# Performance work log

Hardware: AMD Instinct MI355X
Metric: run time of the kernel (lower is better)

## Reference

```python
import jax, jax.numpy as jnp
import numpy as np

N, E, D = 100000, 640000, 128

def setup_inputs() -> dict:
    key = jax.random.key(0)
    ks = jax.random.split(key, 12)
    s = 1.0 / np.sqrt(D)
    sg = 1.0 / np.sqrt(2 * D)
    return {
        "nodes": jax.random.normal(ks[0], (N, D), jnp.float32),
        "globals_": jax.random.normal(ks[1], (1, D), jnp.float32),
        "senders": jax.random.randint(ks[2], (E,), 0, N, jnp.int32),
        "receivers": jax.random.randint(ks[3], (E,), 0, N, jnp.int32),
        "W1_w": jax.random.normal(ks[4], (D, D), jnp.float32) * s,
        "W1_b": jnp.zeros((D,), jnp.float32),
        "W2_w": jax.random.normal(ks[5], (D, D), jnp.float32) * s,
        "W2_b": jnp.zeros((D,), jnp.float32),
        "W3_w": jax.random.normal(ks[6], (D, D), jnp.float32) * s,
        "W3_b": jnp.zeros((D,), jnp.float32),
        "Wg_w": jax.random.normal(ks[7], (2 * D, D), jnp.float32) * sg,
        "Wg_b": jnp.zeros((D,), jnp.float32),
    }


def reference(nodes, globals_, senders, receivers,
              W1_w, W1_b, W2_w, W2_b, W3_w, W3_b, Wg_w, Wg_b):
    n = nodes.shape[0]
    # W1 skip-branch projection
    h = nodes @ W1_w + W1_b                              # [N, D]
    # GraphConvolution: W2 projection + symmetric-normalized sum aggregation
    conv = nodes @ W2_w + W2_b                           # [N, D]
    ones = jnp.ones(senders.shape, conv.dtype)
    send_deg = jax.ops.segment_sum(ones, senders, num_segments=n)
    recv_deg = jax.ops.segment_sum(ones, receivers, num_segments=n)
    conv = conv * jax.lax.rsqrt(jnp.maximum(send_deg, 1.0))[:, None]
    agg = jax.ops.segment_sum(conv[senders], receivers, num_segments=n)  # gather + scatter
    agg = agg * jax.lax.rsqrt(jnp.maximum(recv_deg, 1.0))[:, None]
    h = h + agg
    # global -> node broadcast (globals is not None)
    h = h + (globals_[0:1] @ W3_w + W3_b)
    h = jax.nn.relu(h)
    h = h + nodes                                        # residual
    # global update: aggregate nodes (sum over single graph) + gated residual
    an = jnp.sum(h, axis=0, keepdims=True)               # [1, D]
    g_new = globals_ + jax.nn.relu(jnp.concatenate([an, globals_], axis=-1) @ Wg_w + Wg_b)
    return h, g_new
```

## Files before the change

### kernel.cpp

```cpp
#include <hip/hip_runtime.h>

#define D 128
#define SCH 1024
#define AGGB 2048

typedef __attribute__((ext_vector_type(8))) short short8;
typedef __attribute__((ext_vector_type(4))) float floatx4;

__device__ inline void bf16split(float x, ushort& hi, ushort& lo) {
  unsigned u = __float_as_uint(x);
  unsigned rh = (u + 0x7FFFu + ((u >> 16) & 1u)) & 0xFFFF0000u;
  hi = (ushort)(rh >> 16);
  float fl = x - __uint_as_float(rh);
  unsigned ul = __float_as_uint(fl);
  lo = (ushort)((ul + 0x7FFFu + ((ul >> 16) & 1u)) >> 16);
}

__global__ void k_front(const int* __restrict__ snd, const int* __restrict__ rcv,
                        int* __restrict__ cs, int* __restrict__ cr, int E, int nbE,
                        const float* __restrict__ g, const float* __restrict__ W3,
                        const float* __restrict__ b3, float* __restrict__ gvec) {
  __shared__ float part[256];
  if ((int)blockIdx.x < nbE) {
    const int e = blockIdx.x * 256 + threadIdx.x;
    if (e < E) {
      atomicAdd(cs + snd[e], 1);
      atomicAdd(cr + rcv[e], 1);
    }
    return;
  }
  const int j = threadIdx.x & 127, half = threadIdx.x >> 7;
  float acc = 0.f;
  for (int k = half * 64; k < half * 64 + 64; ++k)
    acc = fmaf(g[k], W3[k * D + j], acc);
  part[threadIdx.x] = acc;
  __syncthreads();
  if (threadIdx.x < D) gvec[j] = b3[j] + part[j] + part[j + 128];
}

__global__ void k_scan(const int* __restrict__ cnt, int* __restrict__ bsum,
                       int* __restrict__ off, int* __restrict__ cursor, int n) {
  __shared__ int sh[256];
  __shared__ int red[4];
  const int t = threadIdx.x, b = blockIdx.x;
  const int base = b * SCH + t * 4;
  int4 v = make_int4(0, 0, 0, 0);
  if (base < n) v = *(const int4*)(cnt + base);
  const int s = v.x + v.y + v.z + v.w;
  sh[t] = s;
  __syncthreads();
  for (int st = 1; st < 256; st <<= 1) {
    const int u = (t >= st) ? sh[t - st] : 0;
    __syncthreads();
    sh[t] += u;
    __syncthreads();
  }
  if (t == 255) atomicExch(bsum + b, sh[255] + 1);
  int pre = 0;
  if (t < b) {
    int x = atomicAdd(bsum + t, 0);
    while (x == 0) {
      __builtin_amdgcn_s_sleep(1);
      x = atomicAdd(bsum + t, 0);
    }
    pre = x - 1;
  }
#pragma unroll
  for (int o = 32; o > 0; o >>= 1) pre += __shfl_down(pre, o, 64);
  if ((t & 63) == 0) red[t >> 6] = pre;
  __syncthreads();
  const int gbase = red[0] + red[1] + red[2] + red[3];
  const int ex = sh[t] - s + gbase;
  if (base < n) {
    const int4 o4 = make_int4(ex, ex + v.x, ex + v.x + v.y, ex + v.x + v.y + v.z);
    *(int4*)(off + base) = o4;
    *(int4*)(cursor + base) = o4;
  }
}

__global__ void k_fill(const int* __restrict__ snd, const int* __restrict__ rcv,
                       int* __restrict__ cursor, int* __restrict__ srt, int E) {
  const int e = blockIdx.x * blockDim.x + threadIdx.x;
  if (e < E) {
    const int p = atomicAdd(cursor + rcv[e], 1);
    srt[p] = snd[e];
  }
}

__global__ __launch_bounds__(256) void k_agg(
    const float* __restrict__ nodes, const int* __restrict__ off,
    int* __restrict__ cnt_recv, const int* __restrict__ cnt_send,
    const int* __restrict__ srt, ushort* __restrict__ yh,
    ushort* __restrict__ yl, int n, const float* __restrict__ W1,
    const float* __restrict__ W2, ushort* __restrict__ wt) {
  if ((int)blockIdx.x >= AGGB) {
    const int id = ((int)blockIdx.x - AGGB) * 256 + threadIdx.x;
    const int mat = id >> 14, idx = id & 16383;
    const int k = idx >> 7, nn = idx & 127;
    const float x = (mat ? W2 : W1)[k * D + nn];
    ushort hi, lo;
    bf16split(x, hi, lo);
    wt[(size_t)mat * 32768 + (size_t)nn * 128 + k] = hi;
    wt[(size_t)mat * 32768 + 16384 + (size_t)nn * 128 + k] = lo;
    return;
  }
  float* cf = (float*)cnt_recv;
  const int hw = threadIdx.x >> 5, ln = threadIdx.x & 31;
  const int ghw = blockIdx.x * 8 + hw;
  const int nhw = AGGB * 8;
  const int c0 = ln * 4;

  for (int r0 = ghw; r0 < n; r0 += 2 * nhw) {
    const int r1 = r0 + nhw;
    const bool has1 = r1 < n;
    const int dg0 = cnt_recv[r0];
    const int o0 = off[r0];
    const int dg1 = has1 ? cnt_recv[r1] : 0;
    const int o1 = has1 ? off[r1] : o0;
    const int safe0 = (dg0 > 0) ? o0 : 0;
    const int safe1 = (dg1 > 0) ? o1 : 0;

    int idx0[8], idx1[8];
#pragma unroll
    for (int j = 0; j < 8; ++j) {
      idx0[j] = srt[safe0 + (j < dg0 ? j : 0)];
      idx1[j] = srt[safe1 + (j < dg1 ? j : 0)];
    }
    float4 g0[8], g1[8];
#pragma unroll
    for (int j = 0; j < 8; ++j)
      g0[j] = *(const float4*)(nodes + (size_t)idx0[j] * D + c0);
#pragma unroll
    for (int j = 0; j < 8; ++j)
      g1[j] = *(const float4*)(nodes + (size_t)idx1[j] * D + c0);
    float rs0[8], rs1[8];
#pragma unroll
    for (int j = 0; j < 8; ++j) {
      rs0[j] = (j < dg0) ? rsqrtf(fmaxf((float)cnt_send[idx0[j]], 1.f)) : 0.f;
      rs1[j] = (j < dg1) ? rsqrtf(fmaxf((float)cnt_send[idx1[j]], 1.f)) : 0.f;
    }

    float sx0 = 0.f, sy0 = 0.f, sz0 = 0.f, sw0 = 0.f, cs0 = 0.f;
    float sx1 = 0.f, sy1 = 0.f, sz1 = 0.f, sw1 = 0.f, cs1 = 0.f;
#pragma unroll
    for (int j = 0; j < 8; ++j) {
      sx0 = fmaf(rs0[j], g0[j].x, sx0);
      sy0 = fmaf(rs0[j], g0[j].y, sy0);
      sz0 = fmaf(rs0[j], g0[j].z, sz0);
      sw0 = fmaf(rs0[j], g0[j].w, sw0);
      cs0 += rs0[j];
      sx1 = fmaf(rs1[j], g1[j].x, sx1);
      sy1 = fmaf(rs1[j], g1[j].y, sy1);
      sz1 = fmaf(rs1[j], g1[j].z, sz1);
      sw1 = fmaf(rs1[j], g1[j].w, sw1);
      cs1 += rs1[j];
    }
    for (int i = 8; i < dg0; ++i) {
      const int s = srt[o0 + i];
      const float r = rsqrtf(fmaxf((float)cnt_send[s], 1.f));
      const float4 c = *(const float4*)(nodes + (size_t)s * D + c0);
      sx0 = fmaf(r, c.x, sx0); sy0 = fmaf(r, c.y, sy0);
      sz0 = fmaf(r, c.z, sz0); sw0 = fmaf(r, c.w, sw0);
      cs0 += r;
    }
    for (int i = 8; i < dg1; ++i) {
      const int s = srt[o1 + i];
      const float r = rsqrtf(fmaxf((float)cnt_send[s], 1.f));
      const float4 c = *(const float4*)(nodes + (size_t)s * D + c0);
      sx1 = fmaf(r, c.x, sx1); sy1 = fmaf(r, c.y, sy1);
      sz1 = fmaf(r, c.z, sz1); sw1 = fmaf(r, c.w, sw1);
      cs1 += r;
    }

    {
      const float rr = rsqrtf(fmaxf((float)dg0, 1.f));
      ushort h0, l0, h1, l1, h2, l2, h3, l3;
      bf16split(sx0 * rr, h0, l0);
      bf16split(sy0 * rr, h1, l1);
      bf16split(sz0 * rr, h2, l2);
      bf16split(sw0 * rr, h3, l3);
      *(ushort4*)(yh + (size_t)r0 * D + c0) = make_ushort4(h0, h1, h2, h3);
      *(ushort4*)(yl + (size_t)r0 * D + c0) = make_ushort4(l0, l1, l2, l3);
      if (ln == 0) cf[r0] = rr * cs0;
    }
    if (has1) {
      const float rr = rsqrtf(fmaxf((float)dg1, 1.f));
      ushort h0, l0, h1, l1, h2, l2, h3, l3;
      bf16split(sx1 * rr, h0, l0);
      bf16split(sy1 * rr, h1, l1);
      bf16split(sz1 * rr, h2, l2);
      bf16split(sw1 * rr, h3, l3);
      *(ushort4*)(yh + (size_t)r1 * D + c0) = make_ushort4(h0, h1, h2, h3);
      *(ushort4*)(yl + (size_t)r1 * D + c0) = make_ushort4(l0, l1, l2, l3);
      if (ln == 0) cf[r1] = rr * cs1;
    }
  }
}

__global__ __launch_bounds__(256, 2) void k_gemm(
    const float* __restrict__ A, const ushort* __restrict__ yh,
    const ushort* __restrict__ yl, const ushort* __restrict__ wt,
    const float* __restrict__ b1, const float* __restrict__ b2,
    const float* __restrict__ gvec, const float* __restrict__ cf,
    float* __restrict__ outH, float* __restrict__ an, int n) {
  __shared__ ushort A1h[64 * 40], A1l[64 * 40], A2h[64 * 40], A2l[64 * 40];
  __shared__ ushort Wh[256 * 40], Wl[256 * 40];
  const int t = threadIdx.x;
  const int row0 = blockIdx.x * 64;
  const int lane = t & 63, w = t >> 6;
  const int m = lane & 15, quad = lane >> 4;

  floatx4 acc[4][2];
#pragma unroll
  for (int i = 0; i < 4; ++i)
#pragma unroll
    for (int j = 0; j < 2; ++j) acc[i][j] = (floatx4)0.f;

  const int arow = t >> 2, akl = (t & 3) * 8;
  const int wcol = t, wmat = wcol >> 7, wn = wcol & 127;
  const int grow = row0 + arow;
  const bool ok = grow < n;

  for (int p = 0; p < 4; ++p) {
    {
      const float* gp = A + (size_t)grow * D + p * 32 + akl;
      float4 v0 = make_float4(0.f, 0.f, 0.f, 0.f), v1 = v0;
      if (ok) {
        v0 = *(const float4*)gp;
        v1 = *(const float4*)(gp + 4);
      }
      ushort h0, l0, h1, l1, h2, l2, h3, l3;
      const int a = arow * 40 + akl;
      bf16split(v0.x, h0, l0); bf16split(v0.y, h1, l1);
      bf16split(v0.z, h2, l2); bf16split(v0.w, h3, l3);
      *(ushort4*)&A1h[a] = make_ushort4(h0, h1, h2, h3);
      *(ushort4*)&A1l[a] = make_ushort4(l0, l1, l2, l3);
      bf16split(v1.x, h0, l0); bf16split(v1.y, h1, l1);
      bf16split(v1.z, h2, l2); bf16split(v1.w, h3, l3);
      *(ushort4*)&A1h[a + 4] = make_ushort4(h0, h1, h2, h3);
      *(ushort4*)&A1l[a + 4] = make_ushort4(l0, l1, l2, l3);
    }
    if (ok) {
      const int a = arow * 40 + akl;
      *(uint4*)&A2h[a] = *(const uint4*)(yh + (size_t)grow * D + p * 32 + akl);
      *(uint4*)&A2l[a] = *(const uint4*)(yl + (size_t)grow * D + p * 32 + akl);
    }
    {
      const ushort* gh = wt + (size_t)wmat * 32768 + (size_t)wn * 128 + p * 32;
      const ushort* gl = gh + 16384;
      const int a = wcol * 40;
#pragma unroll
      for (int c = 0; c < 4; ++c) {
        *(uint4*)&Wh[a + 8 * c] = *(const uint4*)(gh + 8 * c);
        *(uint4*)&Wl[a + 8 * c] = *(const uint4*)(gl + 8 * c);
      }
    }
    __syncthreads();
    short8 a1h[4], a1l[4], a2h[4], a2l[4];
#pragma unroll
    for (int i = 0; i < 4; ++i) {
      const int r = (i * 16 + m) * 40 + quad * 8;
      a1h[i] = *(const short8*)&A1h[r];
      a1l[i] = *(const short8*)&A1l[r];
      a2h[i] = *(const short8*)&A2h[r];
      a2l[i] = *(const short8*)&A2l[r];
    }
#pragma unroll
    for (int j = 0; j < 2; ++j) {
      const int r1 = (w * 32 + j * 16 + m) * 40 + quad * 8;
      const int r2 = (128 + w * 32 + j * 16 + m) * 40 + quad * 8;
      const short8 w1h = *(const short8*)&Wh[r1];
      const short8 w1l = *(const short8*)&Wl[r1];
      const short8 w2h = *(const short8*)&Wh[r2];
      const short8 w2l = *(const short8*)&Wl[r2];
#pragma unroll
      for (int i = 0; i < 4; ++i) {
        floatx4 c = acc[i][j];
        c = __builtin_amdgcn_mfma_f32_16x16x32_bf16(a1h[i], w1h, c, 0, 0, 0);
        c = __builtin_amdgcn_mfma_f32_16x16x32_bf16(a1h[i], w1l, c, 0, 0, 0);
        c = __builtin_amdgcn_mfma_f32_16x16x32_bf16(a1l[i], w1h, c, 0, 0, 0);
        c = __builtin_amdgcn_mfma_f32_16x16x32_bf16(a2h[i], w2h, c, 0, 0, 0);
        c = __builtin_amdgcn_mfma_f32_16x16x32_bf16(a2h[i], w2l, c, 0, 0, 0);
        c = __builtin_amdgcn_mfma_f32_16x16x32_bf16(a2l[i], w2h, c, 0, 0, 0);
        acc[i][j] = c;
      }
    }
    __syncthreads();
  }

  float bb[2], b2c[2];
#pragma unroll
  for (int j = 0; j < 2; ++j) {
    const int col = w * 32 + j * 16 + m;
    bb[j] = b1[col] + gvec[col];
    b2c[j] = b2[col];
  }
  float asum[2] = {0.f, 0.f};
#pragma unroll
  for (int i = 0; i < 4; ++i)
#pragma unroll
    for (int pp = 0; pp < 4; ++pp) {
      const int rg = row0 + i * 16 + quad * 4 + pp;
      if (rg >= n) continue;
      const float crv = cf[rg];
#pragma unroll
      for (int j = 0; j < 2; ++j) {
        const int col = w * 32 + j * 16 + m;
        float v = acc[i][j][pp] + bb[j] + crv * b2c[j];
        v = fmaxf(v, 0.f) + A[(size_t)rg * D + col];
        outH[(size_t)rg * D + col] = v;
        asum[j] += v;
      }
    }
#pragma unroll
  for (int j = 0; j < 2; ++j) {
    float v = asum[j];
    v += __shfl_xor(v, 16);
    v += __shfl_xor(v, 32);
    if (lane < 16) atomicAdd(an + w * 32 + j * 16 + m, v);
  }
}

__global__ void k_gupdate(const float* __restrict__ an, const float* __restrict__ g,
                          const float* __restrict__ Wg, const float* __restrict__ bg,
                          float* __restrict__ gout) {
  __shared__ float part[256];
  const int j = threadIdx.x & 127, half = threadIdx.x >> 7;
  float acc = 0.f;
  if (half == 0) {
    for (int k = 0; k < D; ++k) acc = fmaf(an[k], Wg[k * D + j], acc);
  } else {
    for (int k = 0; k < D; ++k) acc = fmaf(g[k], Wg[(D + k) * D + j], acc);
  }
  part[threadIdx.x] = acc;
  __syncthreads();
  if (threadIdx.x < D)
    gout[j] = g[j] + fmaxf(bg[j] + part[j] + part[j + 128], 0.f);
}

extern "C" void kernel_launch(void* const* d_in, const int* in_sizes, int n_in,
                              void* d_out, int out_size, void* d_ws, size_t ws_size,
                              hipStream_t stream) {
  const float* nodes = (const float*)d_in[0];
  const float* globals_ = (const float*)d_in[1];
  const int* senders = (const int*)d_in[2];
  const int* receivers = (const int*)d_in[3];
  const float* W1_w = (const float*)d_in[4];
  const float* W1_b = (const float*)d_in[5];
  const float* W2_w = (const float*)d_in[6];
  const float* W2_b = (const float*)d_in[7];
  const float* W3_w = (const float*)d_in[8];
  const float* W3_b = (const float*)d_in[9];
  const float* Wg_w = (const float*)d_in[10];
  const float* Wg_b = (const float*)d_in[11];
  const int N = in_sizes[0] / D;
  const int E = in_sizes[2];
  const int nb = (N + SCH - 1) / SCH;
  const int nbE = (E + 255) / 256;

  float* h = (float*)d_out;
  float* gout = h + (size_t)N * D;

  float* ws = (float*)d_ws;
  ushort* yh = (ushort*)ws;
  ushort* yl = yh + (size_t)N * D;
  int* cnt_send = (int*)(yl + (size_t)N * D);
  int* cnt_recv = cnt_send + N;
  int* bsum = cnt_recv + N;
  float* an = (float*)(bsum + 256);
  int* off = (int*)(an + D);
  int* cursor = off + N;
  int* srt = cursor + N;
  float* gvec = (float*)(srt + E);
  ushort* wt = (ushort*)cursor;

  (void)hipMemsetAsync(cnt_send, 0, (size_t)(2 * N + 256 + D) * sizeof(int), stream);

  hipLaunchKernelGGL(k_front, dim3(nbE + 1), dim3(256), 0, stream,
                     senders, receivers, cnt_send, cnt_recv, E, nbE,
                     globals_, W3_w, W3_b, gvec);
  hipLaunchKernelGGL(k_scan, dim3(nb), dim3(256), 0, stream,
                     cnt_recv, bsum, off, cursor, N);
  hipLaunchKernelGGL(k_fill, dim3(nbE), dim3(256), 0, stream,
                     senders, receivers, cursor, srt, E);
  hipLaunchKernelGGL(k_agg, dim3(AGGB + 128), dim3(256), 0, stream,
                     nodes, off, cnt_recv, cnt_send, srt, yh, yl, N,
                     W1_w, W2_w, wt);
  hipLaunchKernelGGL(k_gemm, dim3((N + 63) / 64), dim3(256), 0, stream,
                     nodes, yh, yl, wt, W1_b, W2_b, gvec,
                     (const float*)cnt_recv, h, an, N);
  hipLaunchKernelGGL(k_gupdate, dim3(1), dim3(256), 0, stream, an, globals_,
                     Wg_w, Wg_b, gout);
}
```

Baseline: 362.9 us.

## Pre-split nodes to bf16 hi/lo and drop LDS staging in GEMM

```diff
diff --git a/kernel.cpp b/kernel.cpp
--- a/kernel.cpp
+++ b/kernel.cpp
@@ -19,23 +19,45 @@
 __global__ void k_front(const int* __restrict__ snd, const int* __restrict__ rcv,
                         int* __restrict__ cs, int* __restrict__ cr, int E, int nbE,
                         const float* __restrict__ g, const float* __restrict__ W3,
-                        const float* __restrict__ b3, float* __restrict__ gvec) {
+                        const float* __restrict__ b3, float* __restrict__ gvec,
+                        const float* __restrict__ nodes, ushort* __restrict__ nhl,
+                        int n) {
   __shared__ float part[256];
-  if ((int)blockIdx.x < nbE) {
-    const int e = blockIdx.x * 256 + threadIdx.x;
+  const int b = blockIdx.x;
+  if (b < nbE) {
+    const int e = b * 256 + threadIdx.x;
     if (e < E) {
       atomicAdd(cs + snd[e], 1);
       atomicAdd(cr + rcv[e], 1);
     }
     return;
   }
-  const int j = threadIdx.x & 127, half = threadIdx.x >> 7;
-  float acc = 0.f;
-  for (int k = half * 64; k < half * 64 + 64; ++k)
-    acc = fmaf(g[k], W3[k * D + j], acc);
-  part[threadIdx.x] = acc;
-  __syncthreads();
-  if (threadIdx.x < D) gvec[j] = b3[j] + part[j] + part[j + 128];
+  if (b == nbE) {
+    const int j = threadIdx.x & 127, half = threadIdx.x >> 7;
+    float acc = 0.f;
+    for (int k = half * 64; k < half * 64 + 64; ++k)
+      acc = fmaf(g[k], W3[k * D + j], acc);
+    part[threadIdx.x] = acc;
+    __syncthreads();
+    if (threadIdx.x < D) gvec[j] = b3[j] + part[j] + part[j + 128];
+    return;
+  }
+  const int id = (b - nbE - 1) * 256 + threadIdx.x;
+  if (id >= n * 16) return;
+  const int r = id >> 4, c = (id & 15) * 8;
+  const float* gp = nodes + (size_t)r * D + c;
+  const float4 v0 = *(const float4*)gp;
+  const float4 v1 = *(const float4*)(gp + 4);
+  ushort h0, l0, h1, l1, h2, l2, h3, l3;
+  ushort* ob = nhl + (size_t)r * 256;
+  bf16split(v0.x, h0, l0); bf16split(v0.y, h1, l1);
+  bf16split(v0.z, h2, l2); bf16split(v0.w, h3, l3);
+  *(ushort4*)(ob + c) = make_ushort4(h0, h1, h2, h3);
+  *(ushort4*)(ob + 128 + c) = make_ushort4(l0, l1, l2, l3);
+  bf16split(v1.x, h0, l0); bf16split(v1.y, h1, l1);
+  bf16split(v1.z, h2, l2); bf16split(v1.w, h3, l3);
+  *(ushort4*)(ob + c + 4) = make_ushort4(h0, h1, h2, h3);
+  *(ushort4*)(ob + 128 + c + 4) = make_ushort4(l0, l1, l2, l3);
 }
 
 __global__ void k_scan(const int* __restrict__ cnt, int* __restrict__ bsum,
@@ -197,14 +219,12 @@
   }
 }
 
-__global__ __launch_bounds__(256, 2) void k_gemm(
-    const float* __restrict__ A, const ushort* __restrict__ yh,
+__global__ __launch_bounds__(256, 3) void k_gemm(
+    const float* __restrict__ A, const ushort* nhl, const ushort* __restrict__ yh,
     const ushort* __restrict__ yl, const ushort* __restrict__ wt,
     const float* __restrict__ b1, const float* __restrict__ b2,
     const float* __restrict__ gvec, const float* __restrict__ cf,
-    float* __restrict__ outH, float* __restrict__ an, int n) {
-  __shared__ ushort A1h[64 * 40], A1l[64 * 40], A2h[64 * 40], A2l[64 * 40];
-  __shared__ ushort Wh[256 * 40], Wl[256 * 40];
+    float* outH, float* __restrict__ an, int n) {
   const int t = threadIdx.x;
   const int row0 = blockIdx.x * 64;
   const int lane = t & 63, w = t >> 6;
@@ -216,63 +236,30 @@
 #pragma unroll
     for (int j = 0; j < 2; ++j) acc[i][j] = (floatx4)0.f;
 
-  const int arow = t >> 2, akl = (t & 3) * 8;
-  const int wcol = t, wmat = wcol >> 7, wn = wcol & 127;
-  const int grow = row0 + arow;
-  const bool ok = grow < n;
+  int rr[4];
+#pragma unroll
+  for (int i = 0; i < 4; ++i) rr[i] = min(row0 + i * 16 + m, n - 1);
 
   for (int p = 0; p < 4; ++p) {
-    {
-      const float* gp = A + (size_t)grow * D + p * 32 + akl;
-      float4 v0 = make_float4(0.f, 0.f, 0.f, 0.f), v1 = v0;
-      if (ok) {
-        v0 = *(const float4*)gp;
-        v1 = *(const float4*)(gp + 4);
-      }
-      ushort h0, l0, h1, l1, h2, l2, h3, l3;
-      const int a = arow * 40 + akl;
-      bf16split(v0.x, h0, l0); bf16split(v0.y, h1, l1);
-      bf16split(v0.z, h2, l2); bf16split(v0.w, h3, l3);
-      *(ushort4*)&A1h[a] = make_ushort4(h0, h1, h2, h3);
-      *(ushort4*)&A1l[a] = make_ushort4(l0, l1, l2, l3);
-      bf16split(v1.x, h0, l0); bf16split(v1.y, h1, l1);
-      bf16split(v1.z, h2, l2); bf16split(v1.w, h3, l3);
-      *(ushort4*)&A1h[a + 4] = make_ushort4(h0, h1, h2, h3);
-      *(ushort4*)&A1l[a + 4] = make_ushort4(l0, l1, l2, l3);
-    }
-    if (ok) {
-      const int a = arow * 40 + akl;
-      *(uint4*)&A2h[a] = *(const uint4*)(yh + (size_t)grow * D + p * 32 + akl);
-      *(uint4*)&A2l[a] = *(const uint4*)(yl + (size_t)grow * D + p * 32 + akl);
-    }
-    {
-      const ushort* gh = wt + (size_t)wmat * 32768 + (size_t)wn * 128 + p * 32;
-      const ushort* gl = gh + 16384;
-      const int a = wcol * 40;
-#pragma unroll
-      for (int c = 0; c < 4; ++c) {
-        *(uint4*)&Wh[a + 8 * c] = *(const uint4*)(gh + 8 * c);
-        *(uint4*)&Wl[a + 8 * c] = *(const uint4*)(gl + 8 * c);
-      }
-    }
-    __syncthreads();
+    const int kofs = p * 32 + quad * 8;
     short8 a1h[4], a1l[4], a2h[4], a2l[4];
 #pragma unroll
     for (int i = 0; i < 4; ++i) {
-      const int r = (i * 16 + m) * 40 + quad * 8;
-      a1h[i] = *(const short8*)&A1h[r];
-      a1l[i] = *(const short8*)&A1l[r];
-      a2h[i] = *(const short8*)&A2h[r];
-      a2l[i] = *(const short8*)&A2l[r];
+      const ushort* nb = nhl + (size_t)rr[i] * 256 + kofs;
+      a1h[i] = *(const short8*)nb;
+      a1l[i] = *(const short8*)(nb + 128);
+      const size_t yo = (size_t)rr[i] * D + kofs;
+      a2h[i] = *(const short8*)(yh + yo);
+      a2l[i] = *(const short8*)(yl + yo);
     }
 #pragma unroll
     for (int j = 0; j < 2; ++j) {
-      const int r1 = (w * 32 + j * 16 + m) * 40 + quad * 8;
-      const int r2 = (128 + w * 32 + j * 16 + m) * 40 + quad * 8;
-      const short8 w1h = *(const short8*)&Wh[r1];
-      const short8 w1l = *(const short8*)&Wl[r1];
-      const short8 w2h = *(const short8*)&Wh[r2];
-      const short8 w2l = *(const short8*)&Wl[r2];
+      const int col = w * 32 + j * 16 + m;
+      const ushort* g1 = wt + (size_t)col * 128 + kofs;
+      const short8 w1h = *(const short8*)g1;
+      const short8 w1l = *(const short8*)(g1 + 16384);
+      const short8 w2h = *(const short8*)(g1 + 32768);
+      const short8 w2l = *(const short8*)(g1 + 49152);
 #pragma unroll
       for (int i = 0; i < 4; ++i) {
         floatx4 c = acc[i][j];
@@ -285,8 +272,9 @@
         acc[i][j] = c;
       }
     }
-    __syncthreads();
-  }
+  }
+
+  __syncthreads();
 
   float bb[2], b2c[2];
 #pragma unroll
@@ -357,9 +345,11 @@
   const int E = in_sizes[2];
   const int nb = (N + SCH - 1) / SCH;
   const int nbE = (E + 255) / 256;
+  const int nsb = (N * 16 + 255) / 256;
 
   float* h = (float*)d_out;
   float* gout = h + (size_t)N * D;
+  ushort* nhl = (ushort*)d_out;
 
   float* ws = (float*)d_ws;
   ushort* yh = (ushort*)ws;
@@ -376,9 +366,9 @@
 
   (void)hipMemsetAsync(cnt_send, 0, (size_t)(2 * N + 256 + D) * sizeof(int), stream);
 
-  hipLaunchKernelGGL(k_front, dim3(nbE + 1), dim3(256), 0, stream,
+  hipLaunchKernelGGL(k_front, dim3(nbE + 1 + nsb), dim3(256), 0, stream,
                      senders, receivers, cnt_send, cnt_recv, E, nbE,
-                     globals_, W3_w, W3_b, gvec);
+                     globals_, W3_w, W3_b, gvec, nodes, nhl, N);
   hipLaunchKernelGGL(k_scan, dim3(nb), dim3(256), 0, stream,
                      cnt_recv, bsum, off, cursor, N);
   hipLaunchKernelGGL(k_fill, dim3(nbE), dim3(256), 0, stream,
@@ -387,7 +377,7 @@
                      nodes, off, cnt_recv, cnt_send, srt, yh, yl, N,
                      W1_w, W2_w, wt);
   hipLaunchKernelGGL(k_gemm, dim3((N + 63) / 64), dim3(256), 0, stream,
-                     nodes, yh, yl, wt, W1_b, W2_b, gvec,
+                     nodes, nhl, yh, yl, wt, W1_b, W2_b, gvec,
                      (const float*)cnt_recv, h, an, N);
   hipLaunchKernelGGL(k_gupdate, dim3(1), dim3(256), 0, stream, an, globals_,
                      Wg_w, Wg_b, gout);
```

New measurement: 404.2 us. +11.4%, slower.
